# Performance work log

Measured on AMD Instinct MI355X. Metric: run time of the kernel, lower is better.

Reference implementation:

```python
import jax, jax.numpy as jnp
import numpy as np

TEMPERATURE = 1.0

def _cauchy_kernel(x, y, temperature):
    # pairwise squared distances via Gram trick: ||x_i - y_j||^2
    sq_x = jnp.sum(x * x, axis=1)  # [n]
    sq_y = jnp.sum(y * y, axis=1)  # [m]
    d2 = sq_x[:, None] + sq_y[None, :] - 2.0 * (x @ y.T)
    d2 = jnp.maximum(d2, 0.0)
    return 1.0 / (1.0 + d2 / temperature)


def setup_inputs() -> dict:
    key = jax.random.key(0)
    k1, k2 = jax.random.split(key)
    features = jax.random.normal(k1, (8192, 128), dtype=jnp.float32)
    labels = jax.random.randint(k2, (8192,), 0, 1000, dtype=jnp.int64)
    return {"features": features, "labels": labels}


def reference(features, labels):
    b = features.shape[0] // 2
    z1 = features[:b]
    z2 = features[b:]
    z11 = _cauchy_kernel(z1, z1, TEMPERATURE)  # [b,b]
    z22 = _cauchy_kernel(z2, z2, TEMPERATURE)  # [b,b]
    z12 = _cauchy_kernel(z1, z2, TEMPERATURE)  # [b,b]

    eye = jnp.eye(b, dtype=z11.dtype)
    # positive term: mean log of matched-pair kernel (diagonal of z12)
    pos = jnp.sum(jnp.log(jnp.diagonal(z12))) / b
    # negative terms: row sums over [z11 - I | z12] and [z12^T | z22 - I]
    n1 = jnp.mean(jnp.log((z11 - eye).sum(axis=1) + z12.sum(axis=1)))
    n2 = jnp.mean(jnp.log(z12.sum(axis=0) + (z22 - eye).sum(axis=1)))
    neg = (n1 + n2) / 2.0
    return -(pos - neg)
```

## Files before the change

### kernel.cpp

```cpp
#include <hip/hip_runtime.h>
#include <math.h>

#define N_TOTAL 8192
#define BHALF   4096
#define KDIM    128

typedef __bf16 bf16x8 __attribute__((ext_vector_type(8)));
typedef __bf16 bf16x2 __attribute__((ext_vector_type(2)));
typedef float  f32x4  __attribute__((ext_vector_type(4)));

#define GLOAD_LDS16(GSRC, LDST)                                                \
    __builtin_amdgcn_global_load_lds(                                          \
        (const __attribute__((address_space(1))) void*)(GSRC),                 \
        (__attribute__((address_space(3))) void*)(LDST), 16, 0, 0)

__global__ __launch_bounds__(256) void k_prep(const float* __restrict__ F,
                                              __bf16* __restrict__ Fbf,
                                              float* __restrict__ sq,
                                              float* __restrict__ T) {
    int t = threadIdx.x;
    int row = blockIdx.x * 4 + (t >> 6);
    int l = t & 63;
    const float2* r = (const float2*)(F + (size_t)row * KDIM);
    float2 v = r[l];
    float s = fmaf(v.x, v.x, v.y * v.y);
#pragma unroll
    for (int off = 32; off > 0; off >>= 1) s += __shfl_down(s, off);
    bf16x2 p;
    p[0] = (__bf16)v.x;
    p[1] = (__bf16)v.y;
    ((bf16x2*)(Fbf + (size_t)row * KDIM))[l] = p;
    if (l == 0) {
        sq[row] = s;
        T[row] = 0.0f;
    }
}

__global__ __launch_bounds__(256) void k_pairwise(const __bf16* __restrict__ Fbf,
                                                  const float* __restrict__ sq,
                                                  float* __restrict__ T) {
    int b = blockIdx.x;
    int ti = (int)floorf((129.0f - sqrtf(16641.0f - 8.0f * (float)b)) * 0.5f);
    while (ti * (129 - ti) / 2 > b) --ti;
    while ((ti + 1) * (128 - ti) / 2 <= b) ++ti;
    int tj = ti + (b - ti * (129 - ti) / 2);
    int I = ti * 128, J = tj * 128;
    bool diag = (ti == tj);

    __shared__ __align__(16) __bf16 As[128 * 128];
    __shared__ __align__(16) __bf16 Bs[128 * 128];

    int t = threadIdx.x;
    int w = t >> 6;
    int l = t & 63;
    int wr = w >> 1, wc = w & 1;
    int low = l & 15, kb = l >> 4;

    const __bf16* FA = Fbf + (size_t)I * KDIM;
    const __bf16* FB = Fbf + (size_t)J * KDIM;
#pragma unroll
    for (int it = 0; it < 8; ++it) {
        int f = it * 256 + t;
        int row = f >> 4;
        int sg = f & 15;
        int g = sg ^ (row & 15);
        GLOAD_LDS16(FA + row * KDIM + g * 8, As + (size_t)f * 8);
        GLOAD_LDS16(FB + row * KDIM + g * 8, Bs + (size_t)f * 8);
    }
    __syncthreads();

    const bf16x8* Asg = (const bf16x8*)As;
    const bf16x8* Bsg = (const bf16x8*)Bs;
    f32x4 acc[4][4] = {};
#pragma unroll
    for (int s = 0; s < 4; ++s) {
        int g = s * 4 + kb;
        bf16x8 aF[4], bF[4];
#pragma unroll
        for (int fr = 0; fr < 4; ++fr) {
            int R = wr * 64 + fr * 16 + low;
            aF[fr] = Asg[R * 16 + (g ^ low)];
        }
#pragma unroll
        for (int fc = 0; fc < 4; ++fc) {
            int C = wc * 64 + fc * 16 + low;
            bF[fc] = Bsg[C * 16 + (g ^ low)];
        }
#pragma unroll
        for (int fr = 0; fr < 4; ++fr)
#pragma unroll
            for (int fc = 0; fc < 4; ++fc)
                acc[fr][fc] = __builtin_amdgcn_mfma_f32_16x16x32_bf16(
                    aF[fr], bF[fc], acc[fr][fc], 0, 0, 0);
    }
    __syncthreads();

    float sqi[4][4], sqj[4];
#pragma unroll
    for (int fr = 0; fr < 4; ++fr)
#pragma unroll
        for (int r = 0; r < 4; ++r)
            sqi[fr][r] = sq[I + wr * 64 + fr * 16 + kb * 4 + r];
#pragma unroll
    for (int fc = 0; fc < 4; ++fc)
        sqj[fc] = sq[J + wc * 64 + fc * 16 + low];

    float rowPart[16];
    float colPart[4] = {0.f, 0.f, 0.f, 0.f};
#pragma unroll
    for (int i = 0; i < 16; ++i) rowPart[i] = 0.f;

#pragma unroll
    for (int fr = 0; fr < 4; ++fr) {
#pragma unroll
        for (int fc = 0; fc < 4; ++fc) {
#pragma unroll
            for (int r = 0; r < 4; ++r) {
                float d2 = sqi[fr][r] + sqj[fc] - 2.0f * acc[fr][fc][r];
                d2 = fmaxf(d2, 0.0f);
                float v = __builtin_amdgcn_rcpf(1.0f + d2);
                if (diag && (wr * 64 + fr * 16 + kb * 4 + r) ==
                            (wc * 64 + fc * 16 + low))
                    v = 1.0f;
                rowPart[fr * 4 + r] += v;
                colPart[fc] += v;
            }
        }
    }

    float* rowAcc = (float*)As;
    float* colAcc = (float*)Bs;

#pragma unroll
    for (int i = 0; i < 16; ++i) {
        float x = rowPart[i];
        x += __shfl_xor(x, 1);
        x += __shfl_xor(x, 2);
        x += __shfl_xor(x, 4);
        x += __shfl_xor(x, 8);
        rowPart[i] = x;
    }
    if (low == 0) {
#pragma unroll
        for (int fr = 0; fr < 4; ++fr)
#pragma unroll
            for (int r = 0; r < 4; ++r)
                rowAcc[(wr * 64 + fr * 16 + kb * 4 + r) * 2 + wc] =
                    rowPart[fr * 4 + r];
    }

#pragma unroll
    for (int c = 0; c < 4; ++c) {
        float x = colPart[c];
        x += __shfl_xor(x, 16);
        x += __shfl_xor(x, 32);
        colPart[c] = x;
    }
    if (kb == 0) {
#pragma unroll
        for (int fc = 0; fc < 4; ++fc)
            colAcc[(wc * 64 + fc * 16 + low) * 2 + wr] = colPart[fc];
    }
    __syncthreads();

    if (t < 128) {
        atomicAdd(&T[I + t], rowAcc[t * 2] + rowAcc[t * 2 + 1]);
    } else if (!diag) {
        int c = t - 128;
        atomicAdd(&T[J + c], colAcc[c * 2] + colAcc[c * 2 + 1]);
    }
}

__global__ __launch_bounds__(256) void k_pos(const float* __restrict__ F,
                                             const float* __restrict__ sq,
                                             float* __restrict__ posTerm) {
    int t = threadIdx.x;
    int i = blockIdx.x * 4 + (t >> 6);
    int lane = t & 63;
    const float* r1 = F + (size_t)i * KDIM;
    const float* r2 = F + (size_t)(i + BHALF) * KDIM;
    float d = fmaf(r1[lane], r2[lane], r1[lane + 64] * r2[lane + 64]);
#pragma unroll
    for (int off = 32; off > 0; off >>= 1) d += __shfl_down(d, off);
    if (lane == 0) {
        float d2 = sq[i] + sq[i + BHALF] - 2.0f * d;
        d2 = fmaxf(d2, 0.0f);
        posTerm[i] = -logf(1.0f + d2);
    }
}

__global__ __launch_bounds__(256) void k_final(const float* __restrict__ T,
                                               const float* __restrict__ posTerm,
                                               float* __restrict__ out) {
    int t = threadIdx.x;
    float s1 = 0.f, s2 = 0.f;
    for (int i = t; i < N_TOTAL; i += 256) s1 += logf(T[i] - 1.0f);
    for (int i = t; i < BHALF; i += 256) s2 += posTerm[i];
#pragma unroll
    for (int off = 32; off > 0; off >>= 1) {
        s1 += __shfl_down(s1, off);
        s2 += __shfl_down(s2, off);
    }
    __shared__ float red1[4], red2[4];
    int w = t >> 6, lane = t & 63;
    if (lane == 0) { red1[w] = s1; red2[w] = s2; }
    __syncthreads();
    if (t == 0) {
        float S1 = red1[0] + red1[1] + red1[2] + red1[3];
        float S2 = red2[0] + red2[1] + red2[2] + red2[3];
        out[0] = S1 / (2.0f * (float)BHALF) - S2 / (float)BHALF;
    }
}

extern "C" void kernel_launch(void* const* d_in, const int* in_sizes, int n_in,
                              void* d_out, int out_size, void* d_ws, size_t ws_size,
                              hipStream_t stream) {
    const float* F = (const float*)d_in[0];
    float* out = (float*)d_out;

    char* ws = (char*)d_ws;
    __bf16* Fbf    = (__bf16*)ws;
    float*  sq     = (float*)(ws + (size_t)N_TOTAL * KDIM * 2);
    float*  T      = sq + N_TOTAL;
    float*  posTerm = T + N_TOTAL;

    k_prep<<<N_TOTAL / 4, 256, 0, stream>>>(F, Fbf, sq, T);

    int nTiles = N_TOTAL / 128;
    int nBlocks = nTiles * (nTiles + 1) / 2;
    k_pairwise<<<nBlocks, 256, 0, stream>>>(Fbf, sq, T);

    k_pos<<<BHALF / 4, 256, 0, stream>>>(F, sq, posTerm);

    k_final<<<1, 256, 0, stream>>>(T, posTerm, out);
}
```

Before: 101.9 us.

## Fuse positive term into prep, widen pairwise blocks, parallelize final reduction

The positive-pair term is folded into the prep kernel, which now handles one row from each half. Each block accumulates its part of the loss into the output with an atomic add, so the separate k_pos kernel goes away. The pairwise kernel now runs 512 threads per block, with each wave owning a 32x64 sub-tile. It gets dedicated LDS reduction buffers, which drops the barrier after the MFMA loop, and it no longer overrides the diagonal value. The final log-sum is spread over many blocks with atomics instead of one block. The costs are a memset launch, atomic ordering nondeterminism, and a higher per-block LDS footprint.

```diff
diff --git a/kernel.cpp b/kernel.cpp
--- a/kernel.cpp
+++ b/kernel.cpp
@@ -14,31 +14,55 @@
         (const __attribute__((address_space(1))) void*)(GSRC),                 \
         (__attribute__((address_space(3))) void*)(LDST), 16, 0, 0)
 
-__global__ __launch_bounds__(256) void k_prep(const float* __restrict__ F,
-                                              __bf16* __restrict__ Fbf,
-                                              float* __restrict__ sq,
-                                              float* __restrict__ T) {
+__global__ __launch_bounds__(256) void k_prep_pos(const float* __restrict__ F,
+                                                  __bf16* __restrict__ Fbf,
+                                                  float* __restrict__ sq,
+                                                  float* __restrict__ T,
+                                                  float* __restrict__ out) {
     int t = threadIdx.x;
-    int row = blockIdx.x * 4 + (t >> 6);
-    int l = t & 63;
-    const float2* r = (const float2*)(F + (size_t)row * KDIM);
-    float2 v = r[l];
-    float s = fmaf(v.x, v.x, v.y * v.y);
-#pragma unroll
-    for (int off = 32; off > 0; off >>= 1) s += __shfl_down(s, off);
-    bf16x2 p;
-    p[0] = (__bf16)v.x;
-    p[1] = (__bf16)v.y;
-    ((bf16x2*)(Fbf + (size_t)row * KDIM))[l] = p;
+    int w = t >> 6, l = t & 63;
+    int p = blockIdx.x * 4 + w;
+    const float2* r1 = (const float2*)(F + (size_t)p * KDIM);
+    const float2* r2 = (const float2*)(F + (size_t)(p + BHALF) * KDIM);
+    float2 a = r1[l];
+    float2 c = r2[l];
+
+    float s1 = fmaf(a.x, a.x, a.y * a.y);
+    float s2 = fmaf(c.x, c.x, c.y * c.y);
+    float dp = fmaf(a.x, c.x, a.y * c.y);
+#pragma unroll
+    for (int off = 32; off > 0; off >>= 1) {
+        s1 += __shfl_down(s1, off);
+        s2 += __shfl_down(s2, off);
+        dp += __shfl_down(dp, off);
+    }
+
+    bf16x2 pa, pc;
+    pa[0] = (__bf16)a.x; pa[1] = (__bf16)a.y;
+    pc[0] = (__bf16)c.x; pc[1] = (__bf16)c.y;
+    ((bf16x2*)(Fbf + (size_t)p * KDIM))[l] = pa;
+    ((bf16x2*)(Fbf + (size_t)(p + BHALF) * KDIM))[l] = pc;
+
+    __shared__ float posRed[4];
     if (l == 0) {
-        sq[row] = s;
-        T[row] = 0.0f;
-    }
-}
-
-__global__ __launch_bounds__(256) void k_pairwise(const __bf16* __restrict__ Fbf,
-                                                  const float* __restrict__ sq,
-                                                  float* __restrict__ T) {
+        sq[p] = s1;
+        sq[p + BHALF] = s2;
+        T[p] = 0.0f;
+        T[p + BHALF] = 0.0f;
+        float d2 = fmaxf(s1 + s2 - 2.0f * dp, 0.0f);
+        posRed[w] = logf(1.0f + d2);
+    }
+    __syncthreads();
+    if (t == 0) {
+        float s = posRed[0] + posRed[1] + posRed[2] + posRed[3];
+        atomicAdd(out, s / (float)BHALF);
+    }
+}
+
+__global__ __launch_bounds__(512, 4) void k_pairwise(
+        const __bf16* __restrict__ Fbf,
+        const float* __restrict__ sq,
+        float* __restrict__ T) {
     int b = blockIdx.x;
     int ti = (int)floorf((129.0f - sqrtf(16641.0f - 8.0f * (float)b)) * 0.5f);
     while (ti * (129 - ti) / 2 > b) --ti;
@@ -49,6 +73,8 @@
 
     __shared__ __align__(16) __bf16 As[128 * 128];
     __shared__ __align__(16) __bf16 Bs[128 * 128];
+    __shared__ float rowAcc[128][2];
+    __shared__ float colAcc[128][4];
 
     int t = threadIdx.x;
     int w = t >> 6;
@@ -59,8 +85,8 @@
     const __bf16* FA = Fbf + (size_t)I * KDIM;
     const __bf16* FB = Fbf + (size_t)J * KDIM;
 #pragma unroll
-    for (int it = 0; it < 8; ++it) {
-        int f = it * 256 + t;
+    for (int it = 0; it < 4; ++it) {
+        int f = it * 512 + t;
         int row = f >> 4;
         int sg = f & 15;
         int g = sg ^ (row & 15);
@@ -71,14 +97,14 @@
 
     const bf16x8* Asg = (const bf16x8*)As;
     const bf16x8* Bsg = (const bf16x8*)Bs;
-    f32x4 acc[4][4] = {};
+    f32x4 acc[2][4] = {};
 #pragma unroll
     for (int s = 0; s < 4; ++s) {
         int g = s * 4 + kb;
-        bf16x8 aF[4], bF[4];
-#pragma unroll
-        for (int fr = 0; fr < 4; ++fr) {
-            int R = wr * 64 + fr * 16 + low;
+        bf16x8 aF[2], bF[4];
+#pragma unroll
+        for (int fr = 0; fr < 2; ++fr) {
+            int R = wr * 32 + fr * 16 + low;
             aF[fr] = Asg[R * 16 + (g ^ low)];
         }
 #pragma unroll
@@ -87,31 +113,27 @@
             bF[fc] = Bsg[C * 16 + (g ^ low)];
         }
 #pragma unroll
-        for (int fr = 0; fr < 4; ++fr)
+        for (int fr = 0; fr < 2; ++fr)
 #pragma unroll
             for (int fc = 0; fc < 4; ++fc)
                 acc[fr][fc] = __builtin_amdgcn_mfma_f32_16x16x32_bf16(
                     aF[fr], bF[fc], acc[fr][fc], 0, 0, 0);
     }
-    __syncthreads();
-
-    float sqi[4][4], sqj[4];
-#pragma unroll
-    for (int fr = 0; fr < 4; ++fr)
+
+    float sqi[2][4], sqj[4];
+#pragma unroll
+    for (int fr = 0; fr < 2; ++fr)
 #pragma unroll
         for (int r = 0; r < 4; ++r)
-            sqi[fr][r] = sq[I + wr * 64 + fr * 16 + kb * 4 + r];
+            sqi[fr][r] = sq[I + wr * 32 + fr * 16 + kb * 4 + r];
 #pragma unroll
     for (int fc = 0; fc < 4; ++fc)
         sqj[fc] = sq[J + wc * 64 + fc * 16 + low];
 
-    float rowPart[16];
+    float rowPart[2][4] = {};
     float colPart[4] = {0.f, 0.f, 0.f, 0.f};
 #pragma unroll
-    for (int i = 0; i < 16; ++i) rowPart[i] = 0.f;
-
-#pragma unroll
-    for (int fr = 0; fr < 4; ++fr) {
+    for (int fr = 0; fr < 2; ++fr) {
 #pragma unroll
         for (int fc = 0; fc < 4; ++fc) {
 #pragma unroll
@@ -119,96 +141,58 @@
                 float d2 = sqi[fr][r] + sqj[fc] - 2.0f * acc[fr][fc][r];
                 d2 = fmaxf(d2, 0.0f);
                 float v = __builtin_amdgcn_rcpf(1.0f + d2);
-                if (diag && (wr * 64 + fr * 16 + kb * 4 + r) ==
-                            (wc * 64 + fc * 16 + low))
-                    v = 1.0f;
-                rowPart[fr * 4 + r] += v;
+                rowPart[fr][r] += v;
                 colPart[fc] += v;
             }
         }
     }
 
-    float* rowAcc = (float*)As;
-    float* colAcc = (float*)Bs;
-
-#pragma unroll
-    for (int i = 0; i < 16; ++i) {
-        float x = rowPart[i];
-        x += __shfl_xor(x, 1);
-        x += __shfl_xor(x, 2);
-        x += __shfl_xor(x, 4);
-        x += __shfl_xor(x, 8);
-        rowPart[i] = x;
-    }
-    if (low == 0) {
-#pragma unroll
-        for (int fr = 0; fr < 4; ++fr)
-#pragma unroll
-            for (int r = 0; r < 4; ++r)
-                rowAcc[(wr * 64 + fr * 16 + kb * 4 + r) * 2 + wc] =
-                    rowPart[fr * 4 + r];
-    }
-
-#pragma unroll
-    for (int c = 0; c < 4; ++c) {
-        float x = colPart[c];
+#pragma unroll
+    for (int fr = 0; fr < 2; ++fr)
+#pragma unroll
+        for (int r = 0; r < 4; ++r) {
+            float x = rowPart[fr][r];
+            x += __shfl_xor(x, 1);
+            x += __shfl_xor(x, 2);
+            x += __shfl_xor(x, 4);
+            x += __shfl_xor(x, 8);
+            if (low == 0)
+                rowAcc[wr * 32 + fr * 16 + kb * 4 + r][wc] = x;
+        }
+
+#pragma unroll
+    for (int fc = 0; fc < 4; ++fc) {
+        float x = colPart[fc];
         x += __shfl_xor(x, 16);
         x += __shfl_xor(x, 32);
-        colPart[c] = x;
-    }
-    if (kb == 0) {
-#pragma unroll
-        for (int fc = 0; fc < 4; ++fc)
-            colAcc[(wc * 64 + fc * 16 + low) * 2 + wr] = colPart[fc];
+        if (kb == 0)
+            colAcc[wc * 64 + fc * 16 + low][wr] = x;
     }
     __syncthreads();
 
     if (t < 128) {
-        atomicAdd(&T[I + t], rowAcc[t * 2] + rowAcc[t * 2 + 1]);
-    } else if (!diag) {
+        atomicAdd(&T[I + t], rowAcc[t][0] + rowAcc[t][1]);
+    } else if (t < 256 && !diag) {
         int c = t - 128;
-        atomicAdd(&T[J + c], colAcc[c * 2] + colAcc[c * 2 + 1]);
-    }
-}
-
-__global__ __launch_bounds__(256) void k_pos(const float* __restrict__ F,
-                                             const float* __restrict__ sq,
-                                             float* __restrict__ posTerm) {
-    int t = threadIdx.x;
-    int i = blockIdx.x * 4 + (t >> 6);
-    int lane = t & 63;
-    const float* r1 = F + (size_t)i * KDIM;
-    const float* r2 = F + (size_t)(i + BHALF) * KDIM;
-    float d = fmaf(r1[lane], r2[lane], r1[lane + 64] * r2[lane + 64]);
-#pragma unroll
-    for (int off = 32; off > 0; off >>= 1) d += __shfl_down(d, off);
-    if (lane == 0) {
-        float d2 = sq[i] + sq[i + BHALF] - 2.0f * d;
-        d2 = fmaxf(d2, 0.0f);
-        posTerm[i] = -logf(1.0f + d2);
+        atomicAdd(&T[J + c],
+                  colAcc[c][0] + colAcc[c][1] + colAcc[c][2] + colAcc[c][3]);
     }
 }
 
 __global__ __launch_bounds__(256) void k_final(const float* __restrict__ T,
-                                               const float* __restrict__ posTerm,
                                                float* __restrict__ out) {
     int t = threadIdx.x;
-    float s1 = 0.f, s2 = 0.f;
-    for (int i = t; i < N_TOTAL; i += 256) s1 += logf(T[i] - 1.0f);
-    for (int i = t; i < BHALF; i += 256) s2 += posTerm[i];
-#pragma unroll
-    for (int off = 32; off > 0; off >>= 1) {
-        s1 += __shfl_down(s1, off);
-        s2 += __shfl_down(s2, off);
-    }
-    __shared__ float red1[4], red2[4];
-    int w = t >> 6, lane = t & 63;
-    if (lane == 0) { red1[w] = s1; red2[w] = s2; }
+    int i = blockIdx.x * 256 + t;
+    float s = logf(T[i] - 1.0f);
+#pragma unroll
+    for (int off = 32; off > 0; off >>= 1) s += __shfl_down(s, off);
+    __shared__ float red[4];
+    int w = t >> 6, l = t & 63;
+    if (l == 0) red[w] = s;
     __syncthreads();
     if (t == 0) {
-        float S1 = red1[0] + red1[1] + red1[2] + red1[3];
-        float S2 = red2[0] + red2[1] + red2[2] + red2[3];
-        out[0] = S1 / (2.0f * (float)BHALF) - S2 / (float)BHALF;
+        float S = red[0] + red[1] + red[2] + red[3];
+        atomicAdd(out, S / (2.0f * (float)BHALF));
     }
 }
 
@@ -219,18 +203,17 @@
     float* out = (float*)d_out;
 
     char* ws = (char*)d_ws;
-    __bf16* Fbf    = (__bf16*)ws;
-    float*  sq     = (float*)(ws + (size_t)N_TOTAL * KDIM * 2);
-    float*  T      = sq + N_TOTAL;
-    float*  posTerm = T + N_TOTAL;
-
-    k_prep<<<N_TOTAL / 4, 256, 0, stream>>>(F, Fbf, sq, T);
+    __bf16* Fbf = (__bf16*)ws;
+    float*  sq  = (float*)(ws + (size_t)N_TOTAL * KDIM * 2);
+    float*  T   = sq + N_TOTAL;
+
+    hipMemsetAsync(out, 0, sizeof(float), stream);
+
+    k_prep_pos<<<BHALF / 4, 256, 0, stream>>>(F, Fbf, sq, T, out);
 
     int nTiles = N_TOTAL / 128;
     int nBlocks = nTiles * (nTiles + 1) / 2;
-    k_pairwise<<<nBlocks, 256, 0, stream>>>(Fbf, sq, T);
-
-    k_pos<<<BHALF / 4, 256, 0, stream>>>(F, sq, posTerm);
-
-    k_final<<<1, 256, 0, stream>>>(T, posTerm, out);
-}
+    k_pairwise<<<nBlocks, 512, 0, stream>>>(Fbf, sq, T);
+
+    k_final<<<N_TOTAL / 256, 256, 0, stream>>>(T, out);
+}
```

Result: faster. 98.39 us (-3.4%).
